# Kernel optimization log

Measured on AMD Instinct MI355X. Metric: run time of the kernel, lower is better.

## Reference

```python
import jax, jax.numpy as jnp
import numpy as np

K_MAX, K_MIN = 12.0, 1.0
TEMP = 1.0
STE_ALPHA = 12.0
EPS = 1e-8

DIM, HID, KHID, WHID = 512, 2048, 128, 128
B, N = 8, 1024


def setup_inputs() -> dict:
    key = jax.random.key(0)
    ks = jax.random.split(key, 13)
    def lin(k, fan_in, shape):
        bound = 1.0 / np.sqrt(fan_in)
        return jax.random.uniform(k, shape, jnp.float32, -bound, bound)
    return {
        "x": jax.random.normal(ks[0], (B, N, DIM), jnp.float32),
        "fc1_w": lin(ks[1], DIM, (HID, DIM)),
        "fc1_b": lin(ks[2], DIM, (HID,)),
        "fc2_w": lin(ks[3], HID, (DIM, HID)),
        "fc2_b": lin(ks[4], HID, (DIM,)),
        "k1_w": lin(ks[5], DIM, (KHID, DIM)),
        "k1_b": lin(ks[6], DIM, (KHID,)),
        "k2_w": lin(ks[7], KHID, (3, KHID)),
        "k2_b": lin(ks[8], KHID, (3,)),
        "w1_w": lin(ks[9], DIM, (WHID, DIM)),
        "w1_b": lin(ks[10], DIM, (WHID,)),
        "w2_w": lin(ks[11], WHID, (3, WHID)),
        "w2_b": lin(ks[12], WHID, (3,)),
    }


def adaptive_knn_aggregate(h, k_cont):
    # h: (B,N,C), k_cont: (B,) continuous k in [k_min, k_max]
    sim = jnp.einsum("bnc,bmc->bnm", h, h) / TEMP          # (B,N,N)
    order = jnp.argsort(-sim, axis=-1)                      # descending
    rank = jnp.argsort(order, axis=-1).astype(h.dtype)      # rank 0 = most similar
    # soft top-k gate (STE-style sigmoid around k_cont)
    gate = jax.nn.sigmoid(STE_ALPHA * (k_cont[:, None, None] - (rank + 0.5)))
    attn = jax.nn.softmax(sim, axis=-1) * gate
    attn = attn / (attn.sum(axis=-1, keepdims=True) + EPS)
    return jnp.einsum("bnm,bmc->bnc", attn, h)


def reference(x, fc1_w, fc1_b, fc2_w, fc2_b, k1_w, k1_b, k2_w, k2_b,
              w1_w, w1_b, w2_w, w2_b):
    pooled = x.mean(axis=1)                                 # (B,C)
    # adaptive k values net
    kh = jax.nn.relu(pooled @ k1_w.T + k1_b)
    ratio = jax.nn.sigmoid(kh @ k2_w.T + k2_b)              # (B,3)
    k_cont = K_MIN + ratio * (K_MAX - K_MIN)
    # adaptive branch weights net
    wh = jax.nn.relu(pooled @ w1_w.T + w1_b)
    w = jax.nn.softmax(wh @ w2_w.T + w2_b, axis=-1)         # (B,3)
    # MLP (dropout p=0 -> identity)
    h = jax.nn.relu(x @ fc1_w.T + fc1_b)
    h = h @ fc2_w.T + fc2_b                                 # (B,N,C)
    # three KNN aggregation branches blended by w
    y = sum(adaptive_knn_aggregate(h, k_cont[:, i]) * w[:, i, None, None]
            for i in range(3))
    return y
```

## Files before the change

kernel.cpp:

```cpp
#include <hip/hip_runtime.h>
#include <math.h>

#define DIM_ 512
#define HID_ 2048
#define B_ 8
#define N_ 1024
#define ROWS_ 8192
#define TOPK 16

typedef __attribute__((ext_vector_type(8))) short short8;
typedef __attribute__((ext_vector_type(16))) float float16v;
typedef __attribute__((ext_vector_type(4))) float float4v;

__device__ __forceinline__ float sigm(float x) { return 1.f / (1.f + __expf(-x)); }

__device__ __forceinline__ short f2bf(float f) {
    unsigned u = __float_as_uint(f);
    u += 0x7FFF + ((u >> 16) & 1);
    return (short)(u >> 16);
}

__device__ __forceinline__ float bf2f(unsigned short s) {
    return __uint_as_float((unsigned)s << 16);
}

__device__ __forceinline__ unsigned f2ord(float f) {
    unsigned u = __float_as_uint(f);
    return (u & 0x80000000u) ? ~u : (u | 0x80000000u);
}

__device__ __forceinline__ void gload16(const short* g, short* l) {
    __builtin_amdgcn_global_load_lds(
        (const __attribute__((address_space(1))) void*)g,
        (__attribute__((address_space(3))) void*)l, 16, 0, 0);
}

__global__ __launch_bounds__(512)
void prep_kernel(const float* __restrict__ x, float* __restrict__ part, short* __restrict__ xb,
                 const float* __restrict__ w1, const float* __restrict__ w2,
                 short* __restrict__ o1, short* __restrict__ o2) {
    const int bx = blockIdx.x;
    if (bx < 256) {
        const int b = bx >> 5, chunk = bx & 31;
        const int cg = (threadIdx.x & 127) * 4;
        const int rg = threadIdx.x >> 7;
        const long long rbase = (long long)b * N_ + chunk * 32 + rg * 8;
        const float* xp = x + rbase * DIM_ + cg;
        short* xo = xb + rbase * DIM_ + cg;
        float4 s = make_float4(0.f, 0.f, 0.f, 0.f);
#pragma unroll
        for (int n = 0; n < 8; ++n) {
            const float4 v = *(const float4*)(xp + (long long)n * DIM_);
            s.x += v.x; s.y += v.y; s.z += v.z; s.w += v.w;
            short4 o;
            o.x = f2bf(v.x); o.y = f2bf(v.y); o.z = f2bf(v.z); o.w = f2bf(v.w);
            *(short4*)(xo + (long long)n * DIM_) = o;
        }
        *(float4*)(part + ((long long)bx * 4 + rg) * DIM_ + cg) = s;
    } else {
        const int n4 = HID_ * DIM_ / 4;
        int i = (bx - 256) * 2048 + threadIdx.x;
#pragma unroll
        for (int t = 0; t < 4; ++t, i += 512) {
            const float* in = (i < n4) ? w1 : w2;
            short* out = (i < n4) ? o1 : o2;
            const int j = (i < n4) ? i : (i - n4);
            const float4 v = *(const float4*)(in + (long long)j * 4);
            short4 o;
            o.x = f2bf(v.x); o.y = f2bf(v.y); o.z = f2bf(v.z); o.w = f2bf(v.w);
            *(short4*)(out + (long long)j * 4) = o;
        }
    }
}

__global__ __launch_bounds__(512)
void pool_heads_kernel(const float* __restrict__ part,
                       const float* __restrict__ k1w, const float* __restrict__ k1b,
                       const float* __restrict__ k2w, const float* __restrict__ k2b,
                       const float* __restrict__ w1w, const float* __restrict__ w1b,
                       const float* __restrict__ w2w, const float* __restrict__ w2b,
                       float* __restrict__ kcont, float* __restrict__ wbr) {
    const int b = blockIdx.x;
    const int t = threadIdx.x;
    __shared__ float sp[DIM_];
    __shared__ float kh[128], wh[128];
    __shared__ float wraw[4];
    float s = 0.f;
    for (int g = 0; g < 128; ++g) s += part[((long long)b * 128 + g) * DIM_ + t];
    sp[t] = s * (1.f / 1024.f);
    __syncthreads();

    const int wv = t >> 6, l = t & 63;
    float sv[8];
    {
        const float4 a = *(const float4*)&sp[l * 8];
        const float4 c = *(const float4*)&sp[l * 8 + 4];
        sv[0] = a.x; sv[1] = a.y; sv[2] = a.z; sv[3] = a.w;
        sv[4] = c.x; sv[5] = c.y; sv[6] = c.z; sv[7] = c.w;
    }
#pragma unroll 4
    for (int i = 0; i < 16; ++i) {
        const int r = wv * 16 + i;
        const float4 k0 = *(const float4*)(k1w + (long long)r * DIM_ + l * 8);
        const float4 k1 = *(const float4*)(k1w + (long long)r * DIM_ + l * 8 + 4);
        const float4 q0 = *(const float4*)(w1w + (long long)r * DIM_ + l * 8);
        const float4 q1 = *(const float4*)(w1w + (long long)r * DIM_ + l * 8 + 4);
        float ak = sv[0] * k0.x;
        ak = fmaf(sv[1], k0.y, ak); ak = fmaf(sv[2], k0.z, ak); ak = fmaf(sv[3], k0.w, ak);
        ak = fmaf(sv[4], k1.x, ak); ak = fmaf(sv[5], k1.y, ak);
        ak = fmaf(sv[6], k1.z, ak); ak = fmaf(sv[7], k1.w, ak);
        float aw = sv[0] * q0.x;
        aw = fmaf(sv[1], q0.y, aw); aw = fmaf(sv[2], q0.z, aw); aw = fmaf(sv[3], q0.w, aw);
        aw = fmaf(sv[4], q1.x, aw); aw = fmaf(sv[5], q1.y, aw);
        aw = fmaf(sv[6], q1.z, aw); aw = fmaf(sv[7], q1.w, aw);
#pragma unroll
        for (int d = 32; d > 0; d >>= 1) {
            ak += __shfl_xor(ak, d);
            aw += __shfl_xor(aw, d);
        }
        if (l == 0) {
            kh[r] = fmaxf(ak + k1b[r], 0.f);
            wh[r] = fmaxf(aw + w1b[r], 0.f);
        }
    }
    __syncthreads();
    if (t < 3) {
        float rk = k2b[t], rw = w2b[t];
        for (int k = 0; k < 128; ++k) {
            rk = fmaf(kh[k], k2w[t * 128 + k], rk);
            rw = fmaf(wh[k], w2w[t * 128 + k], rw);
        }
        kcont[b * 3 + t] = 1.f + 11.f * sigm(rk);
        wraw[t] = rw;
    }
    __syncthreads();
    if (t == 0) {
        const float m = fmaxf(wraw[0], fmaxf(wraw[1], wraw[2]));
        const float e0 = __expf(wraw[0] - m), e1 = __expf(wraw[1] - m), e2 = __expf(wraw[2] - m);
        const float inv = 1.f / (e0 + e1 + e2);
        wbr[b * 3 + 0] = e0 * inv;
        wbr[b * 3 + 1] = e1 * inv;
        wbr[b * 3 + 2] = e2 * inv;
    }
}

template<int OUTMODE, int BN, int SWZ>
__global__ __launch_bounds__(256)
void gemm_mfma(const short* __restrict__ A, const short* __restrict__ Bm,
               const float* __restrict__ bias,
               float* __restrict__ outF, short* __restrict__ outB,
               int M, int N, int K, int lda, int ldb,
               long long sA, long long sB, long long sC) {
    constexpr int NJ = BN / 64;
    int bz, mi, ni;
    if (SWZ == 1) {
        const int id = blockIdx.x + gridDim.x * (blockIdx.y + gridDim.y * blockIdx.z);
        bz = id % gridDim.z;
        const int r = id / gridDim.z;
        ni = r % gridDim.x;
        mi = r / gridDim.x;
    } else {
        const int id = blockIdx.x + gridDim.x * blockIdx.y;
        const int numM = gridDim.y;
        const int mg = numM >> 3;
        bz = blockIdx.z;
        mi = (id & 7) * mg + (id >> 3) % mg;
        ni = id / numM;
    }
    A  += (long long)bz * sA;
    Bm += (long long)bz * sB;

    __shared__ short As[128 * 64];
    __shared__ short Bs[BN * 64];

    const int tid = threadIdx.x;
    const int lane = tid & 63;
    const int wv = tid >> 6;
    const int m0 = mi * 128;
    const int n0 = ni * BN;

    const int lrow = lane >> 3;
    const int cg = (lane & 7) ^ lrow;

    const int ml = (wv & 1) * 64;
    const int nl = (wv >> 1) * (BN / 2);
    const int fr = lane & 31;
    const int khh = lane >> 5;

    float16v acc[2][NJ];
#pragma unroll
    for (int i = 0; i < 2; ++i)
#pragma unroll
        for (int j = 0; j < NJ; ++j)
#pragma unroll
            for (int r = 0; r < 16; ++r) acc[i][j][r] = 0.f;

    for (int k0 = 0; k0 < K; k0 += 64) {
        __syncthreads();
#pragma unroll
        for (int i = 0; i < 4; ++i) {
            const int rloc = wv * 32 + i * 8 + lrow;
            gload16(A + (long long)(m0 + rloc) * lda + (k0 + cg * 8),
                    &As[(wv * 32 + i * 8) * 64]);
        }
#pragma unroll
        for (int i = 0; i < BN / 32; ++i) {
            const int rloc = wv * (BN / 4) + i * 8 + lrow;
            gload16(Bm + (long long)(n0 + rloc) * ldb + (k0 + cg * 8),
                    &Bs[(wv * (BN / 4) + i * 8) * 64]);
        }
        __syncthreads();
#pragma unroll
        for (int c = 0; c < 4; ++c) {
            const int ch = c * 2 + khh;
            short8 af[2], bfr[NJ];
#pragma unroll
            for (int i = 0; i < 2; ++i) {
                const int m = ml + i * 32 + fr;
                af[i] = *(const short8*)&As[m * 64 + ((ch ^ (m & 7)) * 8)];
            }
#pragma unroll
            for (int j = 0; j < NJ; ++j) {
                const int n = nl + j * 32 + fr;
                bfr[j] = *(const short8*)&Bs[n * 64 + ((ch ^ (n & 7)) * 8)];
            }
#pragma unroll
            for (int i = 0; i < 2; ++i)
#pragma unroll
                for (int j = 0; j < NJ; ++j)
                    acc[i][j] = __builtin_amdgcn_mfma_f32_32x32x16_bf16(
                        af[i], bfr[j], acc[i][j], 0, 0, 0);
        }
    }

    const long long outOfs = (long long)bz * sC;
#pragma unroll
    for (int i = 0; i < 2; ++i) {
#pragma unroll
        for (int j = 0; j < NJ; ++j) {
            const int ng = n0 + nl + j * 32 + fr;
            float bv = 0.f;
            if (OUTMODE != 2) bv = bias[ng];
#pragma unroll
            for (int r = 0; r < 16; ++r) {
                const int mg2 = m0 + ml + i * 32 + (r & 3) + 8 * (r >> 2) + 4 * khh;
                float v = acc[i][j][r] + bv;
                if (OUTMODE == 0) v = fmaxf(v, 0.f);
                const long long idx = outOfs + (long long)mg2 * N + ng;
                if (OUTMODE == 2) outF[idx] = v;
                else              outB[idx] = f2bf(v);
            }
        }
    }
}

template<int OUTMODE, bool BATCH>
__global__ __launch_bounds__(512, 2)
void gemm256(const short* __restrict__ A, const short* __restrict__ Bm,
             const float* __restrict__ bias, float* __restrict__ outF,
             short* __restrict__ outB, int M, int N, int K, int lda, int ldb,
             int mTiles, long long sA, long long sB, long long sC) {
    __shared__ short As[2][256 * 64];
    __shared__ short Bs[2][256 * 64];

    const int tid = threadIdx.x;
    const int lane = tid & 63;
    const int wv = tid >> 6;
    const int l15 = lane & 15;
    const int kq = lane >> 4;
    const int lr = lane >> 3;
    const int cg = (lane & 7) ^ lr;

    const int id = blockIdx.x;
    const int xcd = id & 7;
    const int r = id >> 3;
    int mi, ni;
    const short* Ag = A;
    const short* Bg = Bm;
    long long cOfs = 0;
    if (BATCH) {
        mi = r % mTiles; ni = r / mTiles;
        Ag += (long long)xcd * sA; Bg += (long long)xcd * sB; cOfs = (long long)xcd * sC;
    } else {
        const int mg = mTiles >> 3;
        mi = xcd * mg + r % mg; ni = r / mg;
    }
    const int m0 = mi * 256, n0 = ni * 256;
    const int wm = wv >> 2, wn = wv & 3;

    float4v acc[8][4];
#pragma unroll
    for (int i = 0; i < 8; ++i)
#pragma unroll
        for (int j = 0; j < 4; ++j)
#pragma unroll
            for (int q = 0; q < 4; ++q) acc[i][j][q] = 0.f;

    const int sB1 = (wv & 3) + (wv >> 2) * 8;

    auto stA = [&](int bf, int s, int k0) {
        gload16(Ag + (long long)(m0 + s * 8 + lr) * lda + (k0 + cg * 8), &As[bf][s * 8 * 64]);
    };
    auto stB = [&](int bf, int s, int k0) {
        gload16(Bg + (long long)(n0 + s * 8 + lr) * ldb + (k0 + cg * 8), &Bs[bf][s * 8 * 64]);
    };
    auto unit0 = [&](int bf, int k0) {
        stA(bf, wv, k0); stA(bf, 16 + wv, k0);
        stB(bf, sB1, k0); stB(bf, 16 + sB1, k0);
    };
    auto unit1 = [&](int bf, int k0) { stA(bf, 8 + wv, k0); stA(bf, 24 + wv, k0); };
    auto unit2 = [&](int bf, int k0) { stB(bf, 4 + sB1, k0); stB(bf, 20 + sB1, k0); };

    auto tile_body = [&](int bf, int k1, bool stage) {
#pragma unroll
        for (int p = 0; p < 4; ++p) {
            const int mq = p & 1, nq = p >> 1;
            short8 af[4][2], bfr[2][2];
#pragma unroll
            for (int f = 0; f < 4; ++f) {
                const int rA = wm * 128 + mq * 64 + f * 16 + l15;
                const int ro = rA * 64, sw = rA & 7;
#pragma unroll
                for (int ks = 0; ks < 2; ++ks)
                    af[f][ks] = *(const short8*)&As[bf][ro + (((ks * 4 + kq) ^ sw) * 8)];
            }
#pragma unroll
            for (int g = 0; g < 2; ++g) {
                const int rB = wn * 64 + nq * 32 + g * 16 + l15;
                const int ro = rB * 64, sw = rB & 7;
#pragma unroll
                for (int ks = 0; ks < 2; ++ks)
                    bfr[g][ks] = *(const short8*)&Bs[bf][ro + (((ks * 4 + kq) ^ sw) * 8)];
            }
            if (stage) {
                if (p == 0) unit0(bf ^ 1, k1);
                else if (p == 1) unit1(bf ^ 1, k1);
                else if (p == 2) unit2(bf ^ 1, k1);
                if (p == 0 || p == 1) asm volatile("s_waitcnt vmcnt(6)" ::: "memory");
                else if (p == 3)      asm volatile("s_waitcnt vmcnt(4)" ::: "memory");
            } else {
                if (p == 0)      asm volatile("s_waitcnt vmcnt(2)" ::: "memory");
                else if (p == 1) asm volatile("s_waitcnt vmcnt(0)" ::: "memory");
            }
            __builtin_amdgcn_s_barrier();
            asm volatile("s_waitcnt lgkmcnt(0)" ::: "memory");
            __builtin_amdgcn_sched_barrier(0);
            __builtin_amdgcn_s_setprio(1);
#pragma unroll
            for (int f = 0; f < 4; ++f)
#pragma unroll
                for (int g = 0; g < 2; ++g)
#pragma unroll
                    for (int ks = 0; ks < 2; ++ks)
                        acc[mq * 4 + f][nq * 2 + g] = __builtin_amdgcn_mfma_f32_16x16x32_bf16(
                            af[f][ks], bfr[g][ks], acc[mq * 4 + f][nq * 2 + g], 0, 0, 0);
            __builtin_amdgcn_s_setprio(0);
            if (stage || p < 3) __builtin_amdgcn_s_barrier();
        }
    };

    const int NT = K >> 6;
    unit0(0, 0);
    __builtin_amdgcn_sched_barrier(0);
    unit1(0, 0);
    __builtin_amdgcn_sched_barrier(0);
    unit2(0, 0);
    asm volatile("s_waitcnt vmcnt(4)" ::: "memory");
    __builtin_amdgcn_s_barrier();

    for (int t = 0; t < NT - 1; ++t)
        tile_body(t & 1, (t + 1) << 6, true);
    tile_body((NT - 1) & 1, 0, false);

#pragma unroll
    for (int mf = 0; mf < 8; ++mf) {
#pragma unroll
        for (int nf = 0; nf < 4; ++nf) {
            const int ng = n0 + wn * 64 + nf * 16 + l15;
            float bv = 0.f;
            if (OUTMODE != 2) bv = bias[ng];
            const int mb = m0 + wm * 128 + mf * 16 + kq * 4;
#pragma unroll
            for (int q = 0; q < 4; ++q) {
                float v = acc[mf][nf][q] + bv;
                if (OUTMODE == 0) v = fmaxf(v, 0.f);
                const long long idx = cOfs + (long long)(mb + q) * N + ng;
                if (OUTMODE == 2) outF[idx] = v;
                else              outB[idx] = f2bf(v);
            }
        }
    }
}

__global__ __launch_bounds__(256)
void topk_agg_kernel(const float* __restrict__ sim,
                     const float* __restrict__ kcont, const float* __restrict__ wbr,
                     const unsigned short* __restrict__ h, float* __restrict__ y) {
    const int wv = threadIdx.x >> 6;
    const int lane = threadIdx.x & 63;
    const int ll = lane & 15;
    const int id = blockIdx.x;
    const int b = id & 7;
    const int row = b * N_ + (id >> 3) * 4 + wv;
    const float* srow = sim + (long long)row * N_;

    const int base = lane * 16;
    float f[16];
#pragma unroll
    for (int q = 0; q < 4; ++q) {
        const float4 v = *(const float4*)(srow + base + q * 4);
        f[q * 4 + 0] = v.x; f[q * 4 + 1] = v.y; f[q * 4 + 2] = v.z; f[q * 4 + 3] = v.w;
    }

    float m = f[0];
#pragma unroll
    for (int j = 1; j < 16; ++j) m = fmaxf(m, f[j]);
#pragma unroll
    for (int d = 32; d > 0; d >>= 1) m = fmaxf(m, __shfl_xor(m, d));
    const float maxv = m;

    float so = 0.f;
#pragma unroll
    for (int j = 0; j < 16; ++j) so += __expf(f[j] - maxv);
#pragma unroll
    for (int d = 32; d > 0; d >>= 1) so += __shfl_xor(so, d);
    const float invden = 1.f / so;

    unsigned key[16];
#pragma unroll
    for (int j = 0; j < 16; ++j)
        key[j] = (f2ord(f[j]) & 0xFFFFFC00u) | (unsigned)(1023 - (base + j));

#pragma unroll
    for (int k = 2; k <= 16; k <<= 1) {
#pragma unroll
        for (int j = k >> 1; j > 0; j >>= 1) {
#pragma unroll
            for (int i = 0; i < 16; ++i) {
                const int l = i ^ j;
                if (l > i) {
                    const bool desc = ((i & k) == 0);
                    const unsigned a = key[i], bk = key[l];
                    const unsigned hi = (a > bk) ? a : bk;
                    const unsigned lo = (a > bk) ? bk : a;
                    key[i] = desc ? hi : lo;
                    key[l] = desc ? lo : hi;
                }
            }
        }
    }

#pragma unroll
    for (int d = 1; d < 64; d <<= 1) {
        unsigned o[16];
#pragma unroll
        for (int i = 0; i < 16; ++i) o[i] = __shfl_xor(key[15 - i], d);
#pragma unroll
        for (int i = 0; i < 16; ++i) key[i] = (key[i] > o[i]) ? key[i] : o[i];
#pragma unroll
        for (int j = 8; j > 0; j >>= 1) {
#pragma unroll
            for (int i = 0; i < 16; ++i) {
                if ((i & j) == 0) {
                    const unsigned a = key[i], bk = key[i | j];
                    key[i]     = (a > bk) ? a : bk;
                    key[i | j] = (a > bk) ? bk : a;
                }
            }
        }
    }

    unsigned k32 = 0;
#pragma unroll
    for (int j = 0; j < 16; ++j) k32 = (ll == j) ? key[j] : k32;
    const int myidx = 1023 - (int)(k32 & 1023u);
    const float myval = srow[myidx];

    unsigned long long kx = ((unsigned long long)f2ord(myval) << 32)
                          | (unsigned)(1023 - myidx);
#pragma unroll
    for (int k = 2; k <= 16; k <<= 1) {
#pragma unroll
        for (int d = k >> 1; d > 0; d >>= 1) {
            const unsigned long long other = __shfl_xor(kx, d);
            const bool keepMax = (((ll & k) != 0) == ((ll & d) != 0));
            const bool mineBig = (kx > other);
            kx = (keepMax == mineBig) ? kx : other;
        }
    }
    const unsigned sord = (unsigned)(kx >> 32);
    const unsigned su = (sord & 0x80000000u) ? (sord & 0x7FFFFFFFu) : ~sord;
    const float sval = __uint_as_float(su);
    const int sidx = 1023 - (int)(kx & 1023u);

    const float kc0 = kcont[b * 3 + 0], kc1 = kcont[b * 3 + 1], kc2 = kcont[b * 3 + 2];
    const float w0 = wbr[b * 3 + 0], w1 = wbr[b * 3 + 1], w2 = wbr[b * 3 + 2];

    const float p = __expf(sval - maxv) * invden;
    const float rr = (float)ll + 0.5f;
    const float g0 = sigm(12.f * (kc0 - rr));
    const float g1 = sigm(12.f * (kc1 - rr));
    const float g2 = sigm(12.f * (kc2 - rr));
    float s0 = p * g0, s1 = p * g1, s2 = p * g2;
#pragma unroll
    for (int d = 1; d < 16; d <<= 1) {
        s0 += __shfl_xor(s0, d);
        s1 += __shfl_xor(s1, d);
        s2 += __shfl_xor(s2, d);
    }
    const float f0 = w0 / (s0 + 1e-8f);
    const float f1 = w1 / (s1 + 1e-8f);
    const float f2 = w2 / (s2 + 1e-8f);
    const float mycoef = p * (f0 * g0 + f1 * g1 + f2 * g2);

    const unsigned short* hbase = h + (long long)b * (N_ * DIM_) + lane * 8;
    const int grp = lane & 48;
    float acc[8] = {0.f, 0.f, 0.f, 0.f, 0.f, 0.f, 0.f, 0.f};
#pragma unroll
    for (int r = 0; r < 16; ++r) {
        const float c = __shfl(mycoef, grp | r);
        const int   i = __shfl(sidx,  grp | r);
        const ushort4 a0 = *(const ushort4*)(hbase + (long long)i * DIM_);
        const ushort4 a1 = *(const ushort4*)(hbase + (long long)i * DIM_ + 4);
        acc[0] = fmaf(c, bf2f(a0.x), acc[0]);
        acc[1] = fmaf(c, bf2f(a0.y), acc[1]);
        acc[2] = fmaf(c, bf2f(a0.z), acc[2]);
        acc[3] = fmaf(c, bf2f(a0.w), acc[3]);
        acc[4] = fmaf(c, bf2f(a1.x), acc[4]);
        acc[5] = fmaf(c, bf2f(a1.y), acc[5]);
        acc[6] = fmaf(c, bf2f(a1.z), acc[6]);
        acc[7] = fmaf(c, bf2f(a1.w), acc[7]);
    }
    float* yp = y + (long long)row * DIM_ + lane * 8;
    *(float4*)(yp + 0) = make_float4(acc[0], acc[1], acc[2], acc[3]);
    *(float4*)(yp + 4) = make_float4(acc[4], acc[5], acc[6], acc[7]);
}

extern "C" void kernel_launch(void* const* d_in, const int* in_sizes, int n_in,
                              void* d_out, int out_size, void* d_ws, size_t ws_size,
                              hipStream_t stream) {
    const float* x     = (const float*)d_in[0];
    const float* fc1_w = (const float*)d_in[1];
    const float* fc1_b = (const float*)d_in[2];
    const float* fc2_w = (const float*)d_in[3];
    const float* fc2_b = (const float*)d_in[4];
    const float* k1_w  = (const float*)d_in[5];
    const float* k1_b  = (const float*)d_in[6];
    const float* k2_w  = (const float*)d_in[7];
    const float* k2_b  = (const float*)d_in[8];
    const float* w1_w  = (const float*)d_in[9];
    const float* w1_b  = (const float*)d_in[10];
    const float* w2_w  = (const float*)d_in[11];
    const float* w2_b  = (const float*)d_in[12];

    char* ws = (char*)d_ws;
    short* h1b    = (short*)(ws + 0);
    float* simbuf = (float*)(ws + 0);
    short* xb     = (short*)(ws + 33554432);
    short* hb     = (short*)(ws + 67108864);
    short* w1b    = (short*)(ws + 75497472);
    short* w2b    = (short*)(ws + 77594624);
    float* ppart  = (float*)(ws + 79691776);
    float* kcont  = (float*)(ws + 81788928);
    float* wbr    = (float*)(ws + 81789056);

    float* y = (float*)d_out;

    prep_kernel<<<dim3(512), dim3(512), 0, stream>>>(x, ppart, xb, fc1_w, fc2_w, w1b, w2b);
    pool_heads_kernel<<<dim3(B_), dim3(512), 0, stream>>>(ppart, k1_w, k1_b, k2_w, k2_b,
                                                          w1_w, w1_b, w2_w, w2_b, kcont, wbr);
    gemm256<0, false><<<dim3(256), dim3(512), 0, stream>>>(
        xb, w1b, fc1_b, nullptr, h1b, ROWS_, HID_, DIM_, DIM_, DIM_, 32, 0, 0, 0);
    gemm_mfma<1, 64, 2><<<dim3(DIM_ / 64, ROWS_ / 128, 1), dim3(256), 0, stream>>>(
        h1b, w2b, fc2_b, nullptr, hb, ROWS_, DIM_, HID_, HID_, HID_, 0, 0, 0);
    gemm_mfma<2, 128, 1><<<dim3(N_ / 128, N_ / 128, B_), dim3(256), 0, stream>>>(
        hb, hb, nullptr, simbuf, nullptr, N_, N_, DIM_, DIM_, DIM_,
        (long long)N_ * DIM_, (long long)N_ * DIM_, (long long)N_ * N_);
    topk_agg_kernel<<<dim3(ROWS_ / 4), dim3(256), 0, stream>>>(
        simbuf, kcont, wbr, (const unsigned short*)hb, y);
}
```

Baseline: 214.8 us.

## Replace cross-lane bitonic top-k merge with iterative wave-max extraction and DPP reductions

The per-row top-16 selection no longer does a 6-stage cross-lane bitonic merge of packed keys followed by a re-read and a 16-lane sort. Instead each lane sorts its 16 values locally, and the wave then extracts the global maximum 16 times using DPP max reductions, a ballot to find the owning lane, and a register shift in that lane. Row max, softmax denominator and gate sums now use DPP/readlane reductions in place of shuffles, and the gather loop uses readlane to broadcast coefficients and indices. This removes many ds_swizzle/bpermute shuffles and the extra global reload, but adds 16 serial reduction rounds. Ties are broken by lowest lane rather than the old index-keyed ordering, and the DPP row-broadcast controls used may not behave the same on this architecture.

```diff
diff --git a/kernel.cpp b/kernel.cpp
--- a/kernel.cpp
+++ b/kernel.cpp
@@ -24,9 +24,47 @@
     return __uint_as_float((unsigned)s << 16);
 }
 
-__device__ __forceinline__ unsigned f2ord(float f) {
-    unsigned u = __float_as_uint(f);
-    return (u & 0x80000000u) ? ~u : (u | 0x80000000u);
+template<int CTRL>
+__device__ __forceinline__ float dpp_fmax_t(float v) {
+    const int o = __builtin_amdgcn_update_dpp(__float_as_int(v), __float_as_int(v),
+                                              CTRL, 0xF, 0xF, false);
+    return fmaxf(v, __int_as_float(o));
+}
+__device__ __forceinline__ float wmax64(float v) {
+    v = dpp_fmax_t<0x111>(v);
+    v = dpp_fmax_t<0x112>(v);
+    v = dpp_fmax_t<0x114>(v);
+    v = dpp_fmax_t<0x118>(v);
+    v = dpp_fmax_t<0x142>(v);
+    v = dpp_fmax_t<0x143>(v);
+    return __int_as_float(__builtin_amdgcn_readlane(__float_as_int(v), 63));
+}
+template<int CTRL, int RMASK>
+__device__ __forceinline__ float dpp_fadd0_t(float v) {
+    const int o = __builtin_amdgcn_update_dpp(0, __float_as_int(v), CTRL, RMASK, 0xF, true);
+    return v + __int_as_float(o);
+}
+__device__ __forceinline__ float wsum64(float v) {
+    v = dpp_fadd0_t<0x111, 0xF>(v);
+    v = dpp_fadd0_t<0x112, 0xF>(v);
+    v = dpp_fadd0_t<0x114, 0xF>(v);
+    v = dpp_fadd0_t<0x118, 0xF>(v);
+    v = dpp_fadd0_t<0x142, 0xA>(v);
+    v = dpp_fadd0_t<0x143, 0xC>(v);
+    return __int_as_float(__builtin_amdgcn_readlane(__float_as_int(v), 63));
+}
+template<int CTRL>
+__device__ __forceinline__ float qadd_t(float v) {
+    const int o = __builtin_amdgcn_update_dpp(__float_as_int(v), __float_as_int(v),
+                                              CTRL, 0xF, 0xF, false);
+    return v + __int_as_float(o);
+}
+__device__ __forceinline__ float qsum16(float v) {
+    v = qadd_t<0xB1>(v);
+    v = qadd_t<0x4E>(v);
+    v = qadd_t<0x141>(v);
+    v = qadd_t<0x140>(v);
+    return v;
 }
 
 __device__ __forceinline__ void gload16(const short* g, short* l) {
@@ -412,114 +450,80 @@
         f[q * 4 + 0] = v.x; f[q * 4 + 1] = v.y; f[q * 4 + 2] = v.z; f[q * 4 + 3] = v.w;
     }
 
-    float m = f[0];
-#pragma unroll
-    for (int j = 1; j < 16; ++j) m = fmaxf(m, f[j]);
-#pragma unroll
-    for (int d = 32; d > 0; d >>= 1) m = fmaxf(m, __shfl_xor(m, d));
-    const float maxv = m;
+    float lm = f[0];
+#pragma unroll
+    for (int j = 1; j < 16; ++j) lm = fmaxf(lm, f[j]);
+    const float maxv = wmax64(lm);
 
     float so = 0.f;
 #pragma unroll
     for (int j = 0; j < 16; ++j) so += __expf(f[j] - maxv);
-#pragma unroll
-    for (int d = 32; d > 0; d >>= 1) so += __shfl_xor(so, d);
-    const float invden = 1.f / so;
-
-    unsigned key[16];
-#pragma unroll
-    for (int j = 0; j < 16; ++j)
-        key[j] = (f2ord(f[j]) & 0xFFFFFC00u) | (unsigned)(1023 - (base + j));
-
+    const float invden = 1.f / wsum64(so);
+
+    float sv[16];
+    int   si[16];
+#pragma unroll
+    for (int j = 0; j < 16; ++j) { sv[j] = f[j]; si[j] = base + j; }
 #pragma unroll
     for (int k = 2; k <= 16; k <<= 1) {
 #pragma unroll
-        for (int j = k >> 1; j > 0; j >>= 1) {
+        for (int jj = k >> 1; jj > 0; jj >>= 1) {
 #pragma unroll
             for (int i = 0; i < 16; ++i) {
-                const int l = i ^ j;
+                const int l = i ^ jj;
                 if (l > i) {
                     const bool desc = ((i & k) == 0);
-                    const unsigned a = key[i], bk = key[l];
-                    const unsigned hi = (a > bk) ? a : bk;
-                    const unsigned lo = (a > bk) ? bk : a;
-                    key[i] = desc ? hi : lo;
-                    key[l] = desc ? lo : hi;
+                    const bool sw = desc ? (sv[i] < sv[l]) : (sv[i] > sv[l]);
+                    const float tv = sw ? sv[l] : sv[i];
+                    sv[l] = sw ? sv[i] : sv[l];
+                    sv[i] = tv;
+                    const int ti = sw ? si[l] : si[i];
+                    si[l] = sw ? si[i] : si[l];
+                    si[i] = ti;
                 }
             }
         }
     }
 
-#pragma unroll
-    for (int d = 1; d < 64; d <<= 1) {
-        unsigned o[16];
-#pragma unroll
-        for (int i = 0; i < 16; ++i) o[i] = __shfl_xor(key[15 - i], d);
-#pragma unroll
-        for (int i = 0; i < 16; ++i) key[i] = (key[i] > o[i]) ? key[i] : o[i];
-#pragma unroll
-        for (int j = 8; j > 0; j >>= 1) {
-#pragma unroll
-            for (int i = 0; i < 16; ++i) {
-                if ((i & j) == 0) {
-                    const unsigned a = key[i], bk = key[i | j];
-                    key[i]     = (a > bk) ? a : bk;
-                    key[i | j] = (a > bk) ? bk : a;
-                }
-            }
-        }
-    }
-
-    unsigned k32 = 0;
-#pragma unroll
-    for (int j = 0; j < 16; ++j) k32 = (ll == j) ? key[j] : k32;
-    const int myidx = 1023 - (int)(k32 & 1023u);
-    const float myval = srow[myidx];
-
-    unsigned long long kx = ((unsigned long long)f2ord(myval) << 32)
-                          | (unsigned)(1023 - myidx);
-#pragma unroll
-    for (int k = 2; k <= 16; k <<= 1) {
-#pragma unroll
-        for (int d = k >> 1; d > 0; d >>= 1) {
-            const unsigned long long other = __shfl_xor(kx, d);
-            const bool keepMax = (((ll & k) != 0) == ((ll & d) != 0));
-            const bool mineBig = (kx > other);
-            kx = (keepMax == mineBig) ? kx : other;
-        }
-    }
-    const unsigned sord = (unsigned)(kx >> 32);
-    const unsigned su = (sord & 0x80000000u) ? (sord & 0x7FFFFFFFu) : ~sord;
-    const float sval = __uint_as_float(su);
-    const int sidx = 1023 - (int)(kx & 1023u);
+    float rv = -3.0e38f;
+    int   ri = 0;
+#pragma unroll
+    for (int r = 0; r < TOPK; ++r) {
+        const float gm = wmax64(sv[0]);
+        const unsigned long long bal = __ballot(sv[0] == gm);
+        const int owner = __ffsll(bal) - 1;
+        const int oidx = __builtin_amdgcn_readlane(si[0], owner);
+        if (ll == r) { rv = gm; ri = oidx; }
+        if (lane == owner) {
+#pragma unroll
+            for (int j = 0; j < 15; ++j) { sv[j] = sv[j + 1]; si[j] = si[j + 1]; }
+            sv[15] = -3.0e38f;
+        }
+    }
 
     const float kc0 = kcont[b * 3 + 0], kc1 = kcont[b * 3 + 1], kc2 = kcont[b * 3 + 2];
     const float w0 = wbr[b * 3 + 0], w1 = wbr[b * 3 + 1], w2 = wbr[b * 3 + 2];
 
-    const float p = __expf(sval - maxv) * invden;
+    const float p = __expf(rv - maxv) * invden;
     const float rr = (float)ll + 0.5f;
     const float g0 = sigm(12.f * (kc0 - rr));
     const float g1 = sigm(12.f * (kc1 - rr));
     const float g2 = sigm(12.f * (kc2 - rr));
-    float s0 = p * g0, s1 = p * g1, s2 = p * g2;
-#pragma unroll
-    for (int d = 1; d < 16; d <<= 1) {
-        s0 += __shfl_xor(s0, d);
-        s1 += __shfl_xor(s1, d);
-        s2 += __shfl_xor(s2, d);
-    }
+    const float s0 = qsum16(p * g0);
+    const float s1 = qsum16(p * g1);
+    const float s2 = qsum16(p * g2);
     const float f0 = w0 / (s0 + 1e-8f);
     const float f1 = w1 / (s1 + 1e-8f);
     const float f2 = w2 / (s2 + 1e-8f);
     const float mycoef = p * (f0 * g0 + f1 * g1 + f2 * g2);
 
     const unsigned short* hbase = h + (long long)b * (N_ * DIM_) + lane * 8;
-    const int grp = lane & 48;
     float acc[8] = {0.f, 0.f, 0.f, 0.f, 0.f, 0.f, 0.f, 0.f};
 #pragma unroll
-    for (int r = 0; r < 16; ++r) {
-        const float c = __shfl(mycoef, grp | r);
-        const int   i = __shfl(sidx,  grp | r);
+    for (int r = 0; r < TOPK; ++r) {
+        const float c = __uint_as_float(
+            (unsigned)__builtin_amdgcn_readlane((int)__float_as_uint(mycoef), r));
+        const int   i = __builtin_amdgcn_readlane(ri, r);
         const ushort4 a0 = *(const ushort4*)(hbase + (long long)i * DIM_);
         const ushort4 a1 = *(const ushort4*)(hbase + (long long)i * DIM_ + 4);
         acc[0] = fmaf(c, bf2f(a0.x), acc[0]);
```

Result: slower. 292.7 us (+36.3%).
